# Kernel optimization log

Measured on AMD Instinct MI355X. Metric: run time of the kernel, lower is better.

## Reference

```python
import jax, jax.numpy as jnp
import numpy as np

NUM_ITER = 64
M_CONST = jnp.array([-1.0, 1.0], dtype=jnp.float32)      # constellation m
ALPHA   = jnp.array([0.5, 0.5], dtype=jnp.float32)       # prior alpha


def setup_inputs() -> dict:
    key = jax.random.key(0)
    k1, k2, k3 = jax.random.split(key, 3)
    B, N_RX, N_TX = 16384, 64, 32
    # channel matrix, scaled ~1/sqrt(N_rx) like a normalized MIMO channel
    Ht = jax.random.normal(k1, (B, N_RX, N_TX), dtype=jnp.float32) / jnp.sqrt(jnp.float32(N_RX))
    yt = jax.random.normal(k2, (B, N_RX), dtype=jnp.float32)
    sigmat0 = jax.random.uniform(k3, (B,), dtype=jnp.float32, minval=0.1, maxval=0.6)
    taui = jnp.ones((NUM_ITER + 1,), dtype=jnp.float32)          # taui0 = 1
    delta = jnp.full((NUM_ITER,), 0.01, dtype=jnp.float32)       # small step size for stability
    return {"yt": yt, "Ht": Ht, "sigmat0": sigmat0, "taui": taui, "delta": delta}


def _cmdnet(yt, Ht, sigmat0, taui, delta):
    m = M_CONST                      # [M]
    log_alpha = jnp.log(ALPHA)       # [M]
    sig2 = (sigmat0 ** 2)[:, None, None]          # [B,1,1]
    B, _, K = Ht.shape
    M = m.shape[0]

    # G0 = zeros broadcast to [B, K, M]
    G = jnp.zeros((B, K, M), dtype=Ht.dtype)
    tau = jnp.abs(taui[0])
    ft = jax.nn.softmax((log_alpha + G) * tau, axis=-1)   # [B,K,M]
    xt = jnp.sum(ft * m, axis=-1)                         # [B,K]

    HH = jnp.einsum('bnk,bnl->bkl', Ht, Ht)               # [B,K,K]
    yH = jnp.einsum('bn,bnk->bk', yt, Ht)                 # [B,K]

    def step(carry, xs):
        G, ft, xt, tau = carry
        d_i, tau_next = xs
        xHH = jnp.einsum('bk,bkl->bl', xt, HH)            # [B,K]
        grad_x = tau * (ft * m - ft * xt[..., None])      # [B,K,M]
        grad_L = sig2 * (1.0 - jnp.exp(-G)) + grad_x * (xHH - yH)[..., None]
        G = G - d_i * grad_L
        tau = jnp.abs(tau_next)
        ft = jax.nn.softmax((log_alpha + G) * tau, axis=-1)
        xt = jnp.sum(ft * m, axis=-1)
        return (G, ft, xt, tau), None

    (G, ft, xt, tau), _ = jax.lax.scan(step, (G, ft, xt, tau), (delta, taui[1:]))
    return ft, xt


def reference(yt, Ht, sigmat0, taui, delta):
    return _cmdnet(yt, Ht, sigmat0, taui, delta)
```

## Files before the change

### kernel.cpp

```cpp
#include <hip/hip_runtime.h>


#define NRX 64
#define KSYM 32

typedef float  f32x16 __attribute__((ext_vector_type(16)));
typedef short  short8 __attribute__((ext_vector_type(8)));
typedef _Float16 h16x2 __attribute__((ext_vector_type(2)));

__device__ __forceinline__ float readlane_f(float v, int lane) {
    return __int_as_float(__builtin_amdgcn_readlane(__float_as_int(v), lane));
}
__device__ __forceinline__ unsigned cvt_pk_bf16(float a, float b) {
    unsigned r;
    asm("v_cvt_pk_bf16_f32 %0, %1, %2" : "=v"(r) : "v"(a), "v"(b));
    return r;
}
__device__ __forceinline__ int cvt_pk_f16(float a, float b) {
    int r;
    asm("v_cvt_pkrtz_f16_f32 %0, %1, %2" : "=v"(r) : "v"(a), "v"(b));
    return r;
}
template <int N>
__device__ __forceinline__ int dpp_ror_i(int v) {
    return __builtin_amdgcn_update_dpp(0, v, 0x120 + N, 0xF, 0xF, true);
}
__device__ __forceinline__ float dot2_f16(int a, int b, float c) {
#if __has_builtin(__builtin_amdgcn_fdot2)
    union { int i; h16x2 h; } ua, ub;
    ua.i = a; ub.i = b;
    return __builtin_amdgcn_fdot2(ua.h, ub.h, c, false);
#else
    float r = c;
    asm("v_dot2_f32_f16 %0, %1, %2, %0" : "+v"(r) : "v"(a), "v"(b));
    return r;
#endif
}
__device__ __forceinline__ float exp2_fast(float x) {
#if __has_builtin(__builtin_amdgcn_exp2f)
    return __builtin_amdgcn_exp2f(x);
#else
    float r; asm("v_exp_f32 %0, %1" : "=v"(r) : "v"(x)); return r;
#endif
}
__device__ __forceinline__ float xor16_f(float x) {
#if __has_builtin(__builtin_amdgcn_permlane16_swap)
    typedef unsigned uint2v __attribute__((ext_vector_type(2)));
    unsigned xi = __float_as_int(x);
    uint2v pr = __builtin_amdgcn_permlane16_swap(xi, xi, false, false);
    return (__uint_as_float(pr[0]) + __uint_as_float(pr[1])) - x;
#else
    return __int_as_float(
        __builtin_amdgcn_ds_swizzle(__float_as_int(x), 0x401F));
#endif
}

union FragU { unsigned u[4]; short8 s; };

__global__ __launch_bounds__(256, 8) void cmdnet_kernel(
    const float* __restrict__ yt,
    const float* __restrict__ Ht,
    const float* __restrict__ sigmat0,
    const float* __restrict__ taui,
    const float* __restrict__ delta,
    float* __restrict__ out_ft,
    float* __restrict__ out_xt,
    int niter)
{
    __shared__ __align__(16) float hhbuf[4][KSYM * KSYM];
    __shared__ __align__(16) float ytL[4][2][NRX];

    const int tid  = threadIdx.x;
    const int w    = tid >> 6;
    const int lane = tid & 63;
    const int k    = lane & 31;
    const int h    = lane >> 5;
    const int hi8  = h * 8;
    const int bb   = blockIdx.x * 8 + w * 2;
    const int b    = bb + h;
    const float LOG2E = 1.4426950408889634f;

    ytL[w][0][lane] = yt[(size_t)bb * NRX + lane];
    ytL[w][1][lane] = yt[(size_t)bb * NRX + NRX + lane];

    float dreg = 0.f, treg = 1.f;
    if (lane < niter) { dreg = delta[lane] * LOG2E; treg = fabsf(taui[lane + 1]); }

    float sig2 = sigmat0[b];
    sig2 *= sig2;

    float yhp0 = 0.f, yhp1 = 0.f;
    f32x16 acc;

    #define MFMA_PASS(S, YHP) do {                                             \
        _Pragma("unroll")                                                      \
        for (int j = 0; j < 16; ++j) acc[j] = 0.f;                             \
        const float* Hb = Ht + ((size_t)(bb + (S))) * (NRX * KSYM);            \
        _Pragma("unroll")                                                      \
        for (int c = 0; c < 4; ++c) {                                          \
            const float* base = Hb + (c * 16 + hi8) * KSYM + k;                \
            float f[8];                                                        \
            _Pragma("unroll")                                                  \
            for (int e = 0; e < 8; ++e) f[e] = base[e * KSYM];                 \
            float4 ya = *reinterpret_cast<const float4*>(&ytL[w][S][c*16+hi8]);\
            float4 yb = *reinterpret_cast<const float4*>(&ytL[w][S][c*16+hi8+4]);\
            YHP = fmaf(ya.x, f[0], YHP); YHP = fmaf(ya.y, f[1], YHP);          \
            YHP = fmaf(ya.z, f[2], YHP); YHP = fmaf(ya.w, f[3], YHP);          \
            YHP = fmaf(yb.x, f[4], YHP); YHP = fmaf(yb.y, f[5], YHP);          \
            YHP = fmaf(yb.z, f[6], YHP); YHP = fmaf(yb.w, f[7], YHP);          \
            FragU hiF, loF;                                                    \
            _Pragma("unroll")                                                  \
            for (int p = 0; p < 4; ++p) {                                      \
                unsigned hp = cvt_pk_bf16(f[2*p], f[2*p+1]);                   \
                float h0 = __uint_as_float(hp << 16);                          \
                float h1 = __uint_as_float(hp & 0xffff0000u);                  \
                loF.u[p] = cvt_pk_bf16(f[2*p] - h0, f[2*p+1] - h1);            \
                hiF.u[p] = hp;                                                 \
            }                                                                  \
            acc = __builtin_amdgcn_mfma_f32_32x32x16_bf16(hiF.s, hiF.s, acc, 0,0,0); \
            acc = __builtin_amdgcn_mfma_f32_32x32x16_bf16(hiF.s, loF.s, acc, 0,0,0); \
            acc = __builtin_amdgcn_mfma_f32_32x32x16_bf16(loF.s, hiF.s, acc, 0,0,0); \
        }                                                                      \
    } while (0)

    #define STORE_ACC() do {                                                   \
        _Pragma("unroll")                                                      \
        for (int j = 0; j < 16; ++j) {                                         \
            int row = (j & 3) + 8 * (j >> 2) + 4 * h;                          \
            hhbuf[w][row * 32 + k] = acc[j];                                   \
        }                                                                      \
    } while (0)

    #define GATHER(DST) do {                                                   \
        const float* rowp = &hhbuf[w][k * 32];                                 \
        const int low4 = k & 15;                                               \
        DST[0] = cvt_pk_f16(0.5f * rowp[k], 0.5f * rowp[k ^ 16]);              \
        GATH(DST, 1)  GATH(DST, 2)  GATH(DST, 3)  GATH(DST, 4)  GATH(DST, 5)  \
        GATH(DST, 6)  GATH(DST, 7)  GATH(DST, 8)  GATH(DST, 9)  GATH(DST, 10) \
        GATH(DST, 11) GATH(DST, 12) GATH(DST, 13) GATH(DST, 14) GATH(DST, 15) \
    } while (0)
    #define GATH(DST, J) {                                                     \
        int idx = dpp_ror_i<J>(low4);                                          \
        DST[J] = cvt_pk_f16(0.5f * rowp[(k & 16) | idx],                       \
                            0.5f * rowp[((k & 16) ^ 16) | idx]); }

    MFMA_PASS(0, yhp0);
    STORE_ACC();
    MFMA_PASS(1, yhp1);
    int gA[16];
    GATHER(gA);
    STORE_ACC();
    int gB[16];
    GATHER(gB);

    int own_pk[16];
    const bool hs = (h != 0);
    #pragma unroll
    for (int j = 0; j < 16; ++j) own_pk[j] = hs ? gB[j] : gA[j];

    float yh0 = yhp0 + __shfl_xor(yhp0, 32, 64);
    float yh1 = yhp1 + __shfl_xor(yhp1, 32, 64);
    float yh  = 0.5f * (hs ? yh1 : yh0);

    float tau = fabsf(taui[0]);
    float Gl0 = 0.f, Gl1 = 0.f;
    float xt = 0.f;

    for (int i = 0; i < niter; ++i) {
        float d2       = readlane_f(dreg, i);
        float tau_next = readlane_f(treg, i);

        float xts = xor16_f(xt);
        int xpk = cvt_pk_f16(xt, xts);

        float a0 = -yh, a1 = 0.f, a2 = 0.f, a3 = 0.f;
        a0 = dot2_f16(own_pk[0], xpk, a0);
        #define STEP(J) {                                                      \
            int xr = dpp_ror_i<J>(xpk);                                        \
            float& aa = ((J) & 3) == 0 ? a0 : ((J) & 3) == 1 ? a1              \
                       : ((J) & 3) == 2 ? a2 : a3;                             \
            aa = dot2_f16(own_pk[J], xr, aa); }
        STEP(1)  STEP(2)  STEP(3)  STEP(4)  STEP(5)
        STEP(6)  STEP(7)  STEP(8)  STEP(9)  STEP(10)
        STEP(11) STEP(12) STEP(13) STEP(14) STEP(15)
        #undef STEP
        float r = (a0 + a1) + (a2 + a3);

        float t  = fmaf(-xt, xt, 1.0f);
        float p  = tau * t * r;
        float e0 = exp2_fast(-Gl0);
        float e1 = exp2_fast(-Gl1);
        float g0 = fmaf(sig2, 1.f - e0, -p);
        float g1 = fmaf(sig2, 1.f - e1,  p);
        Gl0 = fmaf(-d2, g0, Gl0);
        Gl1 = fmaf(-d2, g1, Gl1);

        tau = tau_next;
        float z2 = tau * (Gl1 - Gl0);
        float ez = exp2_fast(-fabsf(z2));
        float sg = __builtin_amdgcn_rcpf(1.f + ez);
        float m  = (1.f - ez) * sg;
        xt = __builtin_copysignf(m, z2);
    }

    float ft1 = fmaf(0.5f, xt, 0.5f);
    float ft0 = 1.f - ft1;
    float2 f2 = make_float2(ft0, ft1);
    reinterpret_cast<float2*>(out_ft)[(size_t)b * KSYM + k] = f2;
    out_xt[(size_t)b * KSYM + k] = xt;
}

extern "C" void kernel_launch(void* const* d_in, const int* in_sizes, int n_in,
                              void* d_out, int out_size, void* d_ws, size_t ws_size,
                              hipStream_t stream) {
    const float* yt    = (const float*)d_in[0];
    const float* Ht    = (const float*)d_in[1];
    const float* sg    = (const float*)d_in[2];
    const float* taui  = (const float*)d_in[3];
    const float* delta = (const float*)d_in[4];
    int B     = in_sizes[2];
    int niter = in_sizes[4];
    float* out    = (float*)d_out;
    float* out_ft = out;
    float* out_xt = out + (size_t)B * 64;

    dim3 grid(B / 8), block(256);
    hipLaunchKernelGGL(cmdnet_kernel, grid, block, 0, stream,
                       yt, Ht, sg, taui, delta, out_ft, out_xt, niter);
}
```

Before: 92.71 us.

## Process four batch items per wavefront with interleaved dual iteration chains

Each wavefront now handles four batch items instead of two, running two independent iteration recurrences (A and B) interleaved in the 64-step loop. The grid is halved and launch bounds drop to 4 blocks per SIMD to allow more registers. The point is to expose instruction-level parallelism in the latency-bound serial loop (DPP, dot2, exp, rcp chains), at the cost of fewer waves in flight and higher register pressure.

```diff
diff --git a/kernel.cpp b/kernel.cpp
--- a/kernel.cpp
+++ b/kernel.cpp
@@ -57,7 +57,7 @@
 
 union FragU { unsigned u[4]; short8 s; };
 
-__global__ __launch_bounds__(256, 8) void cmdnet_kernel(
+__global__ __launch_bounds__(256, 4) void cmdnet_kernel(
     const float* __restrict__ yt,
     const float* __restrict__ Ht,
     const float* __restrict__ sigmat0,
@@ -68,7 +68,7 @@
     int niter)
 {
     __shared__ __align__(16) float hhbuf[4][KSYM * KSYM];
-    __shared__ __align__(16) float ytL[4][2][NRX];
+    __shared__ __align__(16) float ytL[4][4][NRX];
 
     const int tid  = threadIdx.x;
     const int w    = tid >> 6;
@@ -76,20 +76,21 @@
     const int k    = lane & 31;
     const int h    = lane >> 5;
     const int hi8  = h * 8;
-    const int bb   = blockIdx.x * 8 + w * 2;
-    const int b    = bb + h;
+    const int bb   = blockIdx.x * 16 + w * 4;
     const float LOG2E = 1.4426950408889634f;
 
-    ytL[w][0][lane] = yt[(size_t)bb * NRX + lane];
-    ytL[w][1][lane] = yt[(size_t)bb * NRX + NRX + lane];
+    #pragma unroll
+    for (int s = 0; s < 4; ++s)
+        ytL[w][s][lane] = yt[(size_t)(bb + s) * NRX + lane];
 
     float dreg = 0.f, treg = 1.f;
     if (lane < niter) { dreg = delta[lane] * LOG2E; treg = fabsf(taui[lane + 1]); }
 
-    float sig2 = sigmat0[b];
-    sig2 *= sig2;
-
-    float yhp0 = 0.f, yhp1 = 0.f;
+    const int bA = bb + h, bB = bb + 2 + h;
+    float sig2A = sigmat0[bA]; sig2A *= sig2A;
+    float sig2B = sigmat0[bB]; sig2B *= sig2B;
+
+    float yhp0 = 0.f, yhp1 = 0.f, yhp2 = 0.f, yhp3 = 0.f;
     f32x16 acc;
 
     #define MFMA_PASS(S, YHP) do {                                             \
@@ -131,6 +132,10 @@
         }                                                                      \
     } while (0)
 
+    #define GATH(DST, J) {                                                     \
+        int idx = dpp_ror_i<J>(low4);                                          \
+        DST[J] = cvt_pk_f16(0.5f * rowp[(k & 16) | idx],                       \
+                            0.5f * rowp[((k & 16) ^ 16) | idx]); }
     #define GATHER(DST) do {                                                   \
         const float* rowp = &hhbuf[w][k * 32];                                 \
         const int low4 = k & 15;                                               \
@@ -139,75 +144,107 @@
         GATH(DST, 6)  GATH(DST, 7)  GATH(DST, 8)  GATH(DST, 9)  GATH(DST, 10) \
         GATH(DST, 11) GATH(DST, 12) GATH(DST, 13) GATH(DST, 14) GATH(DST, 15) \
     } while (0)
-    #define GATH(DST, J) {                                                     \
-        int idx = dpp_ror_i<J>(low4);                                          \
-        DST[J] = cvt_pk_f16(0.5f * rowp[(k & 16) | idx],                       \
-                            0.5f * rowp[((k & 16) ^ 16) | idx]); }
+
+    const bool hs = (h != 0);
+    int own_pkA[16], own_pkB[16];
 
     MFMA_PASS(0, yhp0);
     STORE_ACC();
     MFMA_PASS(1, yhp1);
-    int gA[16];
-    GATHER(gA);
+    {
+        int g0[16], g1[16];
+        GATHER(g0);
+        STORE_ACC();
+        GATHER(g1);
+        #pragma unroll
+        for (int j = 0; j < 16; ++j) own_pkA[j] = hs ? g1[j] : g0[j];
+    }
+    MFMA_PASS(2, yhp2);
     STORE_ACC();
-    int gB[16];
-    GATHER(gB);
-
-    int own_pk[16];
-    const bool hs = (h != 0);
-    #pragma unroll
-    for (int j = 0; j < 16; ++j) own_pk[j] = hs ? gB[j] : gA[j];
-
-    float yh0 = yhp0 + __shfl_xor(yhp0, 32, 64);
-    float yh1 = yhp1 + __shfl_xor(yhp1, 32, 64);
-    float yh  = 0.5f * (hs ? yh1 : yh0);
+    MFMA_PASS(3, yhp3);
+    {
+        int g2[16], g3[16];
+        GATHER(g2);
+        STORE_ACC();
+        GATHER(g3);
+        #pragma unroll
+        for (int j = 0; j < 16; ++j) own_pkB[j] = hs ? g3[j] : g2[j];
+    }
+
+    float s0 = yhp0 + __shfl_xor(yhp0, 32, 64);
+    float s1 = yhp1 + __shfl_xor(yhp1, 32, 64);
+    float s2 = yhp2 + __shfl_xor(yhp2, 32, 64);
+    float s3 = yhp3 + __shfl_xor(yhp3, 32, 64);
+    float yhA = 0.5f * (hs ? s1 : s0);
+    float yhB = 0.5f * (hs ? s3 : s2);
 
     float tau = fabsf(taui[0]);
-    float Gl0 = 0.f, Gl1 = 0.f;
-    float xt = 0.f;
+    float GA0 = 0.f, GA1 = 0.f, xtA = 0.f;
+    float GB0 = 0.f, GB1 = 0.f, xtB = 0.f;
 
     for (int i = 0; i < niter; ++i) {
         float d2       = readlane_f(dreg, i);
         float tau_next = readlane_f(treg, i);
 
-        float xts = xor16_f(xt);
-        int xpk = cvt_pk_f16(xt, xts);
-
-        float a0 = -yh, a1 = 0.f, a2 = 0.f, a3 = 0.f;
-        a0 = dot2_f16(own_pk[0], xpk, a0);
+        float xtsA = xor16_f(xtA);
+        float xtsB = xor16_f(xtB);
+        int xpkA = cvt_pk_f16(xtA, xtsA);
+        int xpkB = cvt_pk_f16(xtB, xtsB);
+
+        float aA0 = -yhA, aA1 = 0.f, aA2 = 0.f, aA3 = 0.f;
+        float aB0 = -yhB, aB1 = 0.f, aB2 = 0.f, aB3 = 0.f;
+        aA0 = dot2_f16(own_pkA[0], xpkA, aA0);
+        aB0 = dot2_f16(own_pkB[0], xpkB, aB0);
         #define STEP(J) {                                                      \
-            int xr = dpp_ror_i<J>(xpk);                                        \
-            float& aa = ((J) & 3) == 0 ? a0 : ((J) & 3) == 1 ? a1              \
-                       : ((J) & 3) == 2 ? a2 : a3;                             \
-            aa = dot2_f16(own_pk[J], xr, aa); }
+            int xrA = dpp_ror_i<J>(xpkA);                                      \
+            int xrB = dpp_ror_i<J>(xpkB);                                      \
+            float& uA = ((J) & 3) == 0 ? aA0 : ((J) & 3) == 1 ? aA1            \
+                       : ((J) & 3) == 2 ? aA2 : aA3;                           \
+            float& uB = ((J) & 3) == 0 ? aB0 : ((J) & 3) == 1 ? aB1            \
+                       : ((J) & 3) == 2 ? aB2 : aB3;                           \
+            uA = dot2_f16(own_pkA[J], xrA, uA);                                \
+            uB = dot2_f16(own_pkB[J], xrB, uB); }
         STEP(1)  STEP(2)  STEP(3)  STEP(4)  STEP(5)
         STEP(6)  STEP(7)  STEP(8)  STEP(9)  STEP(10)
         STEP(11) STEP(12) STEP(13) STEP(14) STEP(15)
         #undef STEP
-        float r = (a0 + a1) + (a2 + a3);
-
-        float t  = fmaf(-xt, xt, 1.0f);
-        float p  = tau * t * r;
-        float e0 = exp2_fast(-Gl0);
-        float e1 = exp2_fast(-Gl1);
-        float g0 = fmaf(sig2, 1.f - e0, -p);
-        float g1 = fmaf(sig2, 1.f - e1,  p);
-        Gl0 = fmaf(-d2, g0, Gl0);
-        Gl1 = fmaf(-d2, g1, Gl1);
+        float rA = (aA0 + aA1) + (aA2 + aA3);
+        float rB = (aB0 + aB1) + (aB2 + aB3);
+
+        float tA = fmaf(-xtA, xtA, 1.0f);
+        float tB = fmaf(-xtB, xtB, 1.0f);
+        float pA = tau * tA * rA;
+        float pB = tau * tB * rB;
+        float eA0 = exp2_fast(-GA0), eA1 = exp2_fast(-GA1);
+        float eB0 = exp2_fast(-GB0), eB1 = exp2_fast(-GB1);
+        float gA0 = fmaf(sig2A, 1.f - eA0, -pA);
+        float gA1 = fmaf(sig2A, 1.f - eA1,  pA);
+        float gB0 = fmaf(sig2B, 1.f - eB0, -pB);
+        float gB1 = fmaf(sig2B, 1.f - eB1,  pB);
+        GA0 = fmaf(-d2, gA0, GA0);
+        GA1 = fmaf(-d2, gA1, GA1);
+        GB0 = fmaf(-d2, gB0, GB0);
+        GB1 = fmaf(-d2, gB1, GB1);
 
         tau = tau_next;
-        float z2 = tau * (Gl1 - Gl0);
-        float ez = exp2_fast(-fabsf(z2));
-        float sg = __builtin_amdgcn_rcpf(1.f + ez);
-        float m  = (1.f - ez) * sg;
-        xt = __builtin_copysignf(m, z2);
+        float zA = tau * (GA1 - GA0);
+        float zB = tau * (GB1 - GB0);
+        float ezA = exp2_fast(-fabsf(zA));
+        float ezB = exp2_fast(-fabsf(zB));
+        float sgA = __builtin_amdgcn_rcpf(1.f + ezA);
+        float sgB = __builtin_amdgcn_rcpf(1.f + ezB);
+        float mA = (1.f - ezA) * sgA;
+        float mB = (1.f - ezB) * sgB;
+        xtA = __builtin_copysignf(mA, zA);
+        xtB = __builtin_copysignf(mB, zB);
     }
 
-    float ft1 = fmaf(0.5f, xt, 0.5f);
-    float ft0 = 1.f - ft1;
-    float2 f2 = make_float2(ft0, ft1);
-    reinterpret_cast<float2*>(out_ft)[(size_t)b * KSYM + k] = f2;
-    out_xt[(size_t)b * KSYM + k] = xt;
+    float ftA1 = fmaf(0.5f, xtA, 0.5f);
+    float ftB1 = fmaf(0.5f, xtB, 0.5f);
+    reinterpret_cast<float2*>(out_ft)[(size_t)bA * KSYM + k] = make_float2(1.f - ftA1, ftA1);
+    reinterpret_cast<float2*>(out_ft)[(size_t)bB * KSYM + k] = make_float2(1.f - ftB1, ftB1);
+    out_xt[(size_t)bA * KSYM + k] = xtA;
+    out_xt[(size_t)bB * KSYM + k] = xtB;
 }
 
 extern "C" void kernel_launch(void* const* d_in, const int* in_sizes, int n_in,
@@ -224,7 +261,7 @@
     float* out_ft = out;
     float* out_xt = out + (size_t)B * 64;
 
-    dim3 grid(B / 8), block(256);
+    dim3 grid(B / 16), block(256);
     hipLaunchKernelGGL(cmdnet_kernel, grid, block, 0, stream,
                        yt, Ht, sg, taui, delta, out_ft, out_xt, niter);
 }
```

Measured after the change: 81.44 us. -12.2%, faster.
